# Performance work log

Measured on AMD Instinct MI355X. Metric: run time of the kernel, lower is better.

The kernel has to match this reference:

```python
import jax, jax.numpy as jnp
import numpy as np

N = 50000   # nodes
E = 400000  # directed edges (line-graph nodes)
LE = 1600000  # line-graph edges
B = 256     # graphs in batch
F = 64      # n_feats
ED = 16     # edge_dim
NIT = 3     # n_iter
SF = 6 * F  # LinearBlock hidden


def _seg_softmax(vals, seg, num):
    # numerically stable segment softmax (PyG softmax)
    m = jax.ops.segment_max(vals, seg, num_segments=num)
    e = jnp.exp(vals - m[seg])
    s = jax.ops.segment_sum(e, seg, num_segments=num)
    return e / (s[seg] + 1e-16)


def _gat_pool(out, lg_src, lg_dst, batch, gat_W, att_src, att_dst, gat_bias):
    # PyG GATConv(F, 1): heads=1, add_self_loops=True, negative_slope=0.2
    xw = out @ gat_W                       # [E, 1]
    sl = jnp.arange(E, dtype=lg_src.dtype)
    src = jnp.concatenate([lg_src, sl])
    dst = jnp.concatenate([lg_dst, sl])
    a_s = xw[:, 0] * att_src[0]
    a_d = xw[:, 0] * att_dst[0]
    alpha = jax.nn.leaky_relu(a_s[src] + a_d[dst], negative_slope=0.2)
    coef = _seg_softmax(alpha, dst, E)     # softmax over incoming line-edges
    xc = jax.ops.segment_sum(coef[:, None] * xw[src], dst, num_segments=E) + gat_bias  # [E,1]
    # GlobalAttentionPool: segment softmax over batch, then weighted sum pool
    sc = _seg_softmax(xc[:, 0], batch, B)[:, None]
    return jax.ops.segment_sum(out * sc, batch, num_segments=B)  # [B, F]


def _bn(x, g, b):
    # BatchNorm1d in training mode (batch stats, biased var, eps=1e-5)
    m = x.mean(0)
    v = ((x - m) ** 2).mean(0)
    return (x - m) * jax.lax.rsqrt(v + 1e-5) * g + b


def _prelu(x, w):
    return jnp.where(x >= 0, x, w * x)


def _lin_block(x, bn1_g, bn1_b, W1, b1, bn_g, bn_b, pr, W, b, bn5_g, bn5_b, pr5, W5, b5):
    x = _bn(x, bn1_g, bn1_b) @ W1 + b1                       # lin1: [N, 6F]
    h = _prelu(_bn(x, bn_g[0], bn_b[0]), pr[0]) @ W[0] + b[0]  # lin2
    h = _prelu(_bn(h, bn_g[1], bn_b[1]), pr[1]) @ W[1] + b[1]  # lin3
    x = (h + x) / 2
    x = (_prelu(_bn(x, bn_g[2], bn_b[2]), pr[2]) @ W[2] + b[2] + x) / 2  # lin4
    x = _prelu(_bn(x, bn5_g, bn5_b), pr5) @ W5 + b5          # lin5: [N, F]
    return x


def setup_inputs() -> dict:
    key = jax.random.key(0)
    ks = jax.random.split(key, 20)
    def nrm(k, shape, s=0.1):
        return jax.random.normal(k, shape, jnp.float32) * s
    inp = {}
    inp["x"] = jax.random.normal(ks[0], (N, F), jnp.float32)
    inp["edge_attr"] = jax.random.normal(ks[1], (E, ED), jnp.float32)
    inp["edge_index"] = jax.random.randint(ks[2], (2, E), 0, N, jnp.int32)
    inp["line_graph_edge_index"] = jax.random.randint(ks[3], (2, LE), 0, E, jnp.int32)
    inp["edge_index_batch"] = jnp.sort(jax.random.randint(ks[4], (E,), 0, B, jnp.int32))
    inp["W_u"] = nrm(ks[5], (F, F)); inp["W_v"] = nrm(ks[6], (F, F)); inp["W_e"] = nrm(ks[7], (ED, F))
    inp["gat_W"] = nrm(ks[8], (F, 1)); inp["gat_att_src"] = nrm(ks[9], (1,)); inp["gat_att_dst"] = nrm(ks[10], (1,))
    inp["gat_bias"] = jnp.zeros((1,), jnp.float32)
    inp["a"] = nrm(ks[11], (1, F, NIT)); inp["a_bias"] = jnp.zeros((1, 1, NIT), jnp.float32)
    inp["W_gout"] = nrm(ks[12], (F, F)); inp["b_gout"] = jnp.zeros((F,), jnp.float32)
    inp["lb_bn1_g"] = jnp.ones((F,), jnp.float32); inp["lb_bn1_b"] = jnp.zeros((F,), jnp.float32)
    inp["lb_W1"] = nrm(ks[13], (F, SF)); inp["lb_b1"] = jnp.zeros((SF,), jnp.float32)
    inp["lb_bn_g"] = jnp.ones((3, SF), jnp.float32); inp["lb_bn_b"] = jnp.zeros((3, SF), jnp.float32)
    inp["lb_pr"] = jnp.full((3,), 0.25, jnp.float32)
    inp["lb_W"] = nrm(ks[14], (3, SF, SF)); inp["lb_b"] = jnp.zeros((3, SF), jnp.float32)
    inp["lb_bn5_g"] = jnp.ones((SF,), jnp.float32); inp["lb_bn5_b"] = jnp.zeros((SF,), jnp.float32)
    inp["lb_pr5"] = jnp.array(0.25, jnp.float32)
    inp["lb_W5"] = nrm(ks[15], (SF, F)); inp["lb_b5"] = jnp.zeros((F,), jnp.float32)
    return inp


def reference(x, edge_attr, W_u, W_v, W_e, gat_W, gat_att_src, gat_att_dst, gat_bias,
              a, a_bias, W_gout, b_gout,
              lb_bn1_g, lb_bn1_b, lb_W1, lb_b1, lb_bn_g, lb_bn_b, lb_pr, lb_W, lb_b,
              lb_bn5_g, lb_bn5_b, lb_pr5, lb_W5, lb_b5,
              edge_index, line_graph_edge_index, edge_index_batch):
    ei0, ei1 = edge_index[0], edge_index[1]
    lg0, lg1 = line_graph_edge_index[0], line_graph_edge_index[1]
    # initial directed-edge features
    ea = ((x @ W_u)[ei0] + (x @ W_v)[ei1] + edge_attr @ W_e) / 3.0  # [E, F]
    out = ea
    outs, gouts = [], []
    for _ in range(NIT):
        out = ea + jax.ops.segment_sum(out[lg0], lg1, num_segments=E)  # line-graph message passing
        gout = _gat_pool(out, lg0, lg1, edge_index_batch, gat_W, gat_att_src, gat_att_dst, gat_bias)
        outs.append(out)
        gouts.append(jnp.tanh(gout @ W_gout + b_gout))
    out_all = jnp.stack(outs, -1)    # [E, F, NIT]
    gout_all = jnp.stack(gouts, -1)  # [B, F, NIT]
    sc = jax.nn.softmax((gout_all * a).sum(1, keepdims=True) + a_bias, axis=-1)  # [B,1,NIT]
    out = (out_all * sc[edge_index_batch]).sum(-1)  # per-edge gather == repeat_interleave(degree)
    xn = x + jax.ops.segment_sum(out, ei1, num_segments=N)
    return _lin_block(xn, lb_bn1_g, lb_bn1_b, lb_W1, lb_b1, lb_bn_g, lb_bn_b, lb_pr, lb_W, lb_b,
                      lb_bn5_g, lb_bn5_b, lb_pr5, lb_W5, lb_b5)
```

## Files before the change

kernel.cpp:

```cpp
#include <hip/hip_runtime.h>
#include <math.h>

#define NN 50000
#define EE 400000
#define LEE 1600000
#define BBATCH 256
#define FF 64
#define EDD 16
#define NITER 3
#define SFD 384

#define CDIV(a,b) (((a)+(b)-1)/(b))

typedef unsigned short ushort_t;
typedef __attribute__((ext_vector_type(8))) short bf16x8;
typedef __attribute__((ext_vector_type(4))) float f32x4;

__device__ inline float b2f(ushort_t u) { return __uint_as_float(((unsigned)u) << 16); }
__device__ inline ushort_t f2b(float f) {
    unsigned u = __float_as_uint(f);
    return (ushort_t)((u + 0x7fffu + ((u >> 16) & 1u)) >> 16);
}

__global__ void k_hist(const int* __restrict__ idx, int n, int* __restrict__ cnt) {
    int i = blockIdx.x * blockDim.x + threadIdx.x;
    if (i < n) atomicAdd(&cnt[idx[i]], 1);
}
__global__ void k_part(const int* __restrict__ in, int n, int* __restrict__ part) {
    __shared__ int s[256];
    int i = blockIdx.x * 256 + threadIdx.x;
    s[threadIdx.x] = (i < n) ? in[i] : 0;
    __syncthreads();
    for (int off = 128; off > 0; off >>= 1) {
        if (threadIdx.x < off) s[threadIdx.x] += s[threadIdx.x + off];
        __syncthreads();
    }
    if (threadIdx.x == 0) part[blockIdx.x] = s[0];
}
__global__ void k_scan_single(int* __restrict__ a, int n) {
    __shared__ int s[256];
    int v = (threadIdx.x < n) ? a[threadIdx.x] : 0;
    s[threadIdx.x] = v; __syncthreads();
    for (int off = 1; off < 256; off <<= 1) {
        int t = (threadIdx.x >= off) ? s[threadIdx.x - off] : 0;
        __syncthreads(); s[threadIdx.x] += t; __syncthreads();
    }
    if (threadIdx.x < n) a[threadIdx.x] = s[threadIdx.x] - v;
}
__global__ void k_scan_add(int* __restrict__ a, int n, const int* __restrict__ off) {
    __shared__ int s[256];
    int i = blockIdx.x * 256 + threadIdx.x;
    int v = (i < n) ? a[i] : 0;
    s[threadIdx.x] = v; __syncthreads();
    for (int o = 1; o < 256; o <<= 1) {
        int t = (threadIdx.x >= o) ? s[threadIdx.x - o] : 0;
        __syncthreads(); s[threadIdx.x] += t; __syncthreads();
    }
    if (i < n) a[i] = s[threadIdx.x] - v + off[blockIdx.x];
}
__global__ void k_scan_out(const int* __restrict__ in, int n, const int* __restrict__ boff,
                           int* __restrict__ out) {
    __shared__ int s[256];
    int i = blockIdx.x * 256 + threadIdx.x;
    int v = (i < n) ? in[i] : 0;
    s[threadIdx.x] = v; __syncthreads();
    for (int o = 1; o < 256; o <<= 1) {
        int t = (threadIdx.x >= o) ? s[threadIdx.x - o] : 0;
        __syncthreads(); s[threadIdx.x] += t; __syncthreads();
    }
    if (i < n) out[i] = s[threadIdx.x] - v + boff[blockIdx.x];
    if (i == n - 1) out[n] = s[threadIdx.x] + boff[blockIdx.x];
}
__global__ void k_fill_lg(const int* __restrict__ lg, const int* __restrict__ rowptr,
                          int* __restrict__ cnt, int* __restrict__ srcidx) {
    int i = blockIdx.x * blockDim.x + threadIdx.x;
    if (i >= LEE) return;
    int d = lg[LEE + i];
    int pos = rowptr[d] + atomicAdd(&cnt[d], 1);
    srcidx[pos] = lg[i];
}
__global__ void k_fill_n(const int* __restrict__ ei, const int* __restrict__ rowptr,
                         int* __restrict__ cnt, int* __restrict__ nidx) {
    int i = blockIdx.x * blockDim.x + threadIdx.x;
    if (i >= EE) return;
    int d = ei[EE + i];
    int pos = rowptr[d] + atomicAdd(&cnt[d], 1);
    nidx[pos] = i;
}


__global__ void k_node_mm(const float* __restrict__ x, const float* __restrict__ Wu,
                          const float* __restrict__ Wv, ushort_t* __restrict__ xu,
                          ushort_t* __restrict__ xv) {
    __shared__ float su[64 * 64];
    __shared__ float sv[64 * 64];
    int tid = threadIdx.x;
    for (int i = tid; i < 64 * 64; i += blockDim.x) { su[i] = Wu[i]; sv[i] = Wv[i]; }
    __syncthreads();
    int row = blockIdx.x * 4 + (tid >> 6);
    int f = tid & 63;
    if (row >= NN) return;
    const float* xr = x + (long long)row * 64;
    float au = 0.f, av = 0.f;
    #pragma unroll
    for (int k = 0; k < 64; ++k) {
        float xv_ = xr[k];
        au += xv_ * su[k * 64 + f];
        av += xv_ * sv[k * 64 + f];
    }
    xu[(long long)row * 64 + f] = f2b(au);
    xv[(long long)row * 64 + f] = f2b(av);
}

__global__ void k_ea_b16(const ushort_t* __restrict__ xu, const ushort_t* __restrict__ xv,
                         const float* __restrict__ eattr, const float* __restrict__ We,
                         const int* __restrict__ ei, ushort_t* __restrict__ eab) {
    __shared__ float swe[16 * 64];
    int tid = threadIdx.x;
    for (int i = tid; i < 1024; i += 256) swe[i] = We[i];
    __syncthreads();
    int e = blockIdx.x * 8 + (tid >> 5);
    int f2 = (tid & 31) * 2;
    if (e >= EE) return;
    int s = ei[e];
    int d = ei[EE + e];
    unsigned us = *(const unsigned*)&xu[(long long)s * 64 + f2];
    unsigned ud = *(const unsigned*)&xv[(long long)d * 64 + f2];
    const float* ar = eattr + (long long)e * 16;
    float a0 = 0.f, a1 = 0.f;
    #pragma unroll
    for (int k = 0; k < 16; ++k) {
        float w = ar[k];
        a0 += w * swe[k * 64 + f2];
        a1 += w * swe[k * 64 + f2 + 1];
    }
    float v0 = (b2f((ushort_t)us) + b2f((ushort_t)ud) + a0) * (1.0f / 3.0f);
    float v1 = (b2f((ushort_t)(us >> 16)) + b2f((ushort_t)(ud >> 16)) + a1) * (1.0f / 3.0f);
    *(unsigned*)&eab[(long long)e * 64 + f2] = (unsigned)f2b(v0) | ((unsigned)f2b(v1) << 16);
}

__global__ void k_mp_gather(const ushort_t* __restrict__ prev,
                            const ushort_t* __restrict__ eab,
                            const int* __restrict__ rowptr, const int* __restrict__ srcidx,
                            const float* __restrict__ gatW,
                            ushort_t* __restrict__ outb, float* __restrict__ xw) {
    int tid = threadIdx.x;
    int d = blockIdx.x * 8 + (tid >> 5);
    int f2 = (tid & 31) * 2;
    if (d >= EE) return;
    unsigned ue = *(const unsigned*)&eab[(long long)d * 64 + f2];
    float a0 = b2f((ushort_t)ue), a1 = b2f((ushort_t)(ue >> 16));
    int p0 = rowptr[d], p1 = rowptr[d + 1];
    int j = p0;
    for (; j + 4 <= p1; j += 4) {
        int s0 = srcidx[j], s1 = srcidx[j + 1], s2 = srcidx[j + 2], s3 = srcidx[j + 3];
        unsigned u0 = *(const unsigned*)&prev[(long long)s0 * 64 + f2];
        unsigned u1 = *(const unsigned*)&prev[(long long)s1 * 64 + f2];
        unsigned u2 = *(const unsigned*)&prev[(long long)s2 * 64 + f2];
        unsigned u3 = *(const unsigned*)&prev[(long long)s3 * 64 + f2];
        a0 += (b2f((ushort_t)u0) + b2f((ushort_t)u1)) + (b2f((ushort_t)u2) + b2f((ushort_t)u3));
        a1 += (b2f((ushort_t)(u0 >> 16)) + b2f((ushort_t)(u1 >> 16))) +
              (b2f((ushort_t)(u2 >> 16)) + b2f((ushort_t)(u3 >> 16)));
    }
    for (; j < p1; ++j) {
        unsigned u0 = *(const unsigned*)&prev[(long long)srcidx[j] * 64 + f2];
        a0 += b2f((ushort_t)u0);
        a1 += b2f((ushort_t)(u0 >> 16));
    }
    *(unsigned*)&outb[(long long)d * 64 + f2] = (unsigned)f2b(a0) | ((unsigned)f2b(a1) << 16);
    float w = a0 * gatW[f2] + a1 * gatW[f2 + 1];
    #pragma unroll
    for (int o = 16; o > 0; o >>= 1) w += __shfl_down(w, o, 32);
    if ((tid & 31) == 0) xw[d] = w;
}

__global__ void k_gat_fused(const float* __restrict__ xw,
                            const int* __restrict__ rowptr, const int* __restrict__ srcidx,
                            const float* __restrict__ att_s, const float* __restrict__ att_d,
                            const float* __restrict__ gbias, float* __restrict__ xc) {
    int e = blockIdx.x * blockDim.x + threadIdx.x;
    if (e >= EE) return;
    float as = att_s[0], ad = att_d[0];
    float xwd = xw[e];
    float adt = xwd * ad;
    float aself = xwd * as + adt;
    if (aself < 0.f) aself *= 0.2f;
    int p0 = rowptr[e], p1 = rowptr[e + 1];
    float m = aself;
    for (int j = p0; j < p1; ++j) {
        float a = xw[srcidx[j]] * as + adt;
        if (a < 0.f) a *= 0.2f;
        m = fmaxf(m, a);
    }
    float ssum = expf(aself - m);
    float wsum = ssum * xwd;
    for (int j = p0; j < p1; ++j) {
        float xs = xw[srcidx[j]];
        float a = xs * as + adt;
        if (a < 0.f) a *= 0.2f;
        float ev = expf(a - m);
        ssum += ev;
        wsum += ev * xs;
    }
    xc[e] = wsum / (ssum + 1e-16f) + gbias[0];
}

__global__ void k_batchptr(const int* __restrict__ batch, int* __restrict__ bptr) {
    int e = blockIdx.x * blockDim.x + threadIdx.x;
    if (e >= EE) return;
    int b = batch[e];
    int bp = (e == 0) ? -1 : batch[e - 1];
    for (int q = bp + 1; q <= b; ++q) bptr[q] = e;
    if (e == EE - 1)
        for (int q = b + 1; q <= BBATCH; ++q) bptr[q] = EE;
}

__global__ void k_pool(const float* __restrict__ xc, const ushort_t* __restrict__ out,
                       const int* __restrict__ bptr, float* __restrict__ gout) {
    int b = blockIdx.x;
    int p0 = bptr[b], p1 = bptr[b + 1];
    __shared__ float red[256];
    int tid = threadIdx.x;
    float mx = -INFINITY;
    for (int e = p0 + tid; e < p1; e += 256) mx = fmaxf(mx, xc[e]);
    red[tid] = mx; __syncthreads();
    for (int s = 128; s > 0; s >>= 1) { if (tid < s) red[tid] = fmaxf(red[tid], red[tid + s]); __syncthreads(); }
    float m = red[0]; __syncthreads();
    float sm = 0.f;
    for (int e = p0 + tid; e < p1; e += 256) sm += expf(xc[e] - m);
    red[tid] = sm; __syncthreads();
    for (int s = 128; s > 0; s >>= 1) { if (tid < s) red[tid] += red[tid + s]; __syncthreads(); }
    float ssum = red[0] + 1e-16f; __syncthreads();
    int f = tid & 63, chunk = tid >> 6;
    float acc = 0.f;
    for (int e = p0 + chunk; e < p1; e += 4) {
        float w = expf(xc[e] - m);
        acc += w * b2f(out[(long long)e * 64 + f]);
    }
    red[tid] = acc; __syncthreads();
    if (chunk == 0) {
        float tot = red[f] + red[64 + f] + red[128 + f] + red[192 + f];
        gout[b * 64 + f] = tot / ssum;
    }
}

__global__ void k_gout_mm(const float* __restrict__ gout, const float* __restrict__ Wg,
                          const float* __restrict__ bg, float* __restrict__ gt) {
    __shared__ float sw[64 * 64];
    int tid = threadIdx.x;
    for (int i = tid; i < 4096; i += blockDim.x) sw[i] = Wg[i];
    __syncthreads();
    int row = blockIdx.x * 4 + (tid >> 6);
    int f = tid & 63;
    if (row >= BBATCH) return;
    const float* gr = gout + row * 64;
    float acc = bg[f];
    #pragma unroll
    for (int k = 0; k < 64; ++k) acc += gr[k] * sw[k * 64 + f];
    gt[row * 64 + f] = tanhf(acc);
}

__global__ void k_att(const float* __restrict__ g0, const float* __restrict__ g1,
                      const float* __restrict__ g2, const float* __restrict__ a,
                      const float* __restrict__ abias, float* __restrict__ sc) {
    int b = blockIdx.x;
    int f = threadIdx.x;
    float v0 = g0[b * 64 + f] * a[f * 3 + 0];
    float v1 = g1[b * 64 + f] * a[f * 3 + 1];
    float v2 = g2[b * 64 + f] * a[f * 3 + 2];
    #pragma unroll
    for (int o = 32; o > 0; o >>= 1) {
        v0 += __shfl_down(v0, o, 64);
        v1 += __shfl_down(v1, o, 64);
        v2 += __shfl_down(v2, o, 64);
    }
    if (f == 0) {
        float s0 = v0 + abias[0], s1 = v1 + abias[1], s2 = v2 + abias[2];
        float m = fmaxf(s0, fmaxf(s1, s2));
        float e0 = expf(s0 - m), e1 = expf(s1 - m), e2 = expf(s2 - m);
        float inv = 1.0f / (e0 + e1 + e2);
        sc[b * 3 + 0] = e0 * inv; sc[b * 3 + 1] = e1 * inv; sc[b * 3 + 2] = e2 * inv;
    }
}

__global__ void k_comb(ushort_t* __restrict__ o1, const ushort_t* __restrict__ o2,
                       const ushort_t* __restrict__ o3, const float* __restrict__ sc,
                       const int* __restrict__ batch) {
    long long idx = (long long)blockIdx.x * blockDim.x + threadIdx.x;
    if (idx >= (long long)EE * 64) return;
    int e = (int)(idx >> 6);
    int b = batch[e];
    float v = b2f(o1[idx]) * sc[b * 3] + b2f(o2[idx]) * sc[b * 3 + 1] + b2f(o3[idx]) * sc[b * 3 + 2];
    o1[idx] = f2b(v);
}

__global__ void k_node_gather(const ushort_t* __restrict__ comb, const int* __restrict__ nrow,
                              const int* __restrict__ nidx, const float* __restrict__ x,
                              ushort_t* __restrict__ xnb) {
    int tid = threadIdx.x;
    int n = blockIdx.x * 4 + (tid >> 6);
    int f = tid & 63;
    if (n >= NN) return;
    float acc = x[(long long)n * 64 + f];
    int p0 = nrow[n], p1 = nrow[n + 1];
    int j = p0;
    for (; j + 4 <= p1; j += 4) {
        int e0 = nidx[j], e1 = nidx[j + 1], e2 = nidx[j + 2], e3 = nidx[j + 3];
        float v0 = b2f(comb[(long long)e0 * 64 + f]);
        float v1 = b2f(comb[(long long)e1 * 64 + f]);
        float v2 = b2f(comb[(long long)e2 * 64 + f]);
        float v3 = b2f(comb[(long long)e3 * 64 + f]);
        acc += (v0 + v1) + (v2 + v3);
    }
    for (; j < p1; ++j) acc += b2f(comb[(long long)nidx[j] * 64 + f]);
    xnb[(long long)n * 64 + f] = f2b(acc);
}

__global__ void k_colstats_b16(const ushort_t* __restrict__ X, int ncols, int nrows,
                               float* __restrict__ csum, float* __restrict__ csumsq) {
    int c = threadIdx.x;
    int rpb = CDIV(nrows, (int)gridDim.x);
    int r0 = blockIdx.x * rpb;
    int r1 = min(r0 + rpb, nrows);
    float s = 0.f, s2 = 0.f;
    for (int r = r0; r < r1; ++r) {
        float v = b2f(X[(long long)r * ncols + c]);
        s += v; s2 += v * v;
    }
    atomicAdd(&csum[c], s);
    atomicAdd(&csumsq[c], s2);
}

__global__ void k_wtrans(const float* __restrict__ W, int K, int M, ushort_t* __restrict__ Wt) {
    __shared__ ushort_t tile[32][33];
    int kb = blockIdx.y * 32, mb = blockIdx.x * 32;
    int tx = threadIdx.x & 31, ty = threadIdx.x >> 5;
    for (int dy = ty; dy < 32; dy += 8) {
        int k = kb + dy, m = mb + tx;
        tile[dy][tx] = (k < K && m < M) ? f2b(W[(long long)k * M + m]) : (ushort_t)0;
    }
    __syncthreads();
    for (int dy = ty; dy < 32; dy += 8) {
        int m = mb + dy, k = kb + tx;
        if (m < M && k < K) Wt[(long long)m * K + k] = tile[tx][dy];
    }
}

template<int KK, int WR, int WC>
__global__ __launch_bounds__(256) void k_gemm_fused(
    const ushort_t* __restrict__ A, const ushort_t* __restrict__ Wt,
    const float* __restrict__ bias, const ushort_t* __restrict__ resb,
    const float* __restrict__ csum, const float* __restrict__ csumsq,
    const float* __restrict__ g, const float* __restrict__ bb,
    const float* __restrict__ pr, float scale, int nrows, int M,
    ushort_t* __restrict__ Cb, float* __restrict__ Cf,
    float* __restrict__ osum, float* __restrict__ osumsq) {
    constexpr int RT = WR * 64;
    __shared__ ushort_t sA[RT][36];
    __shared__ float sScl[KK], sOff[KK];
    int tid = threadIdx.x;
    int wave = tid >> 6, lane = tid & 63;
    int l16 = lane & 15, klo = lane >> 4;
    int wrow = wave / WC, wcol = wave % WC;
    long long rowBase = (long long)blockIdx.x * RT;
    int colBase = blockIdx.y * (WC * 64);
    float prs = pr ? pr[0] : 1.0f;
    const float invn = 1.0f / (float)NN;
    for (int c = tid; c < KK; c += 256) {
        float mean = csum[c] * invn;
        float var = csumsq[c] * invn - mean * mean;
        float scl = rsqrtf(var + 1e-5f) * g[c];
        sScl[c] = scl;
        sOff[c] = bb[c] - mean * scl;
    }
    __syncthreads();
    f32x4 acc[4][4] = {};
    for (int k0 = 0; k0 < KK; k0 += 32) {
        #pragma unroll
        for (int it = 0; it < RT * 32 / (256 * 8); ++it) {
            int idx = (it * 256 + tid) * 8;
            int r = idx >> 5, kk = idx & 31;
            long long gr = rowBase + r;
            uint4 raw = {0u, 0u, 0u, 0u};
            if (gr < nrows) raw = *(const uint4*)&A[gr * KK + k0 + kk];
            unsigned outw[4];
            #pragma unroll
            for (int q = 0; q < 4; ++q) {
                unsigned rw = ((const unsigned*)&raw)[q];
                int c = k0 + kk + q * 2;
                float t0 = b2f((ushort_t)rw) * sScl[c] + sOff[c];
                float t1 = b2f((ushort_t)(rw >> 16)) * sScl[c + 1] + sOff[c + 1];
                if (t0 < 0.f) t0 *= prs;
                if (t1 < 0.f) t1 *= prs;
                outw[q] = (unsigned)f2b(t0) | ((unsigned)f2b(t1) << 16);
            }
            uint2 w0; w0.x = outw[0]; w0.y = outw[1];
            uint2 w1; w1.x = outw[2]; w1.y = outw[3];
            *(uint2*)&sA[r][kk] = w0;
            *(uint2*)&sA[r][kk + 4] = w1;
        }
        __syncthreads();
        bf16x8 bfr[4];
        #pragma unroll
        for (int n = 0; n < 4; ++n) {
            int col = colBase + wcol * 64 + n * 16 + l16;
            bfr[n] = *(const bf16x8*)&Wt[(long long)col * KK + k0 + klo * 8];
        }
        bf16x8 afr[4];
        #pragma unroll
        for (int m = 0; m < 4; ++m) {
            union { uint2 p[2]; bf16x8 v; } u;
            int row = wrow * 64 + m * 16 + l16;
            u.p[0] = *(const uint2*)&sA[row][klo * 8];
            u.p[1] = *(const uint2*)&sA[row][klo * 8 + 4];
            afr[m] = u.v;
        }
        #pragma unroll
        for (int m = 0; m < 4; ++m)
            #pragma unroll
            for (int n = 0; n < 4; ++n)
                acc[m][n] = __builtin_amdgcn_mfma_f32_16x16x32_bf16(afr[m], bfr[n], acc[m][n], 0, 0, 0);
        __syncthreads();
    }
    #pragma unroll
    for (int m = 0; m < 4; ++m) {
        #pragma unroll
        for (int n = 0; n < 4; ++n) {
            int col = colBase + wcol * 64 + n * 16 + l16;
            long long row0 = rowBase + wrow * 64 + m * 16 + klo * 4;
            float bcol = bias[col];
            float s = 0.f, s2 = 0.f;
            #pragma unroll
            for (int r = 0; r < 4; ++r) {
                long long row = row0 + r;
                if (row < nrows) {
                    float v = acc[m][n][r] + bcol;
                    if (resb) v += b2f(resb[row * M + col]);
                    v *= scale;
                    if (Cf) Cf[row * M + col] = v;
                    if (Cb) Cb[row * M + col] = f2b(v);
                    s += v; s2 += v * v;
                }
            }
            if (osum) {
                s += __shfl_down(s, 32, 64);
                s2 += __shfl_down(s2, 32, 64);
                s += __shfl_down(s, 16, 64);
                s2 += __shfl_down(s2, 16, 64);
                if (lane < 16) {
                    atomicAdd(&osum[col], s);
                    atomicAdd(&osumsq[col], s2);
                }
            }
        }
    }
}

extern "C" void kernel_launch(void* const* d_in, const int* in_sizes, int n_in,
                              void* d_out, int out_size, void* d_ws, size_t ws_size,
                              hipStream_t stream) {
    const float* x       = (const float*)d_in[0];
    const float* eattr   = (const float*)d_in[1];
    const int*   ei      = (const int*)d_in[2];
    const int*   lg      = (const int*)d_in[3];
    const int*   batch   = (const int*)d_in[4];
    const float* W_u     = (const float*)d_in[5];
    const float* W_v     = (const float*)d_in[6];
    const float* W_e     = (const float*)d_in[7];
    const float* gat_W   = (const float*)d_in[8];
    const float* att_s   = (const float*)d_in[9];
    const float* att_d   = (const float*)d_in[10];
    const float* gat_b   = (const float*)d_in[11];
    const float* a_att   = (const float*)d_in[12];
    const float* a_bias  = (const float*)d_in[13];
    const float* W_gout  = (const float*)d_in[14];
    const float* b_gout  = (const float*)d_in[15];
    const float* bn1_g   = (const float*)d_in[16];
    const float* bn1_b   = (const float*)d_in[17];
    const float* lb_W1   = (const float*)d_in[18];
    const float* lb_b1   = (const float*)d_in[19];
    const float* lb_bn_g = (const float*)d_in[20];
    const float* lb_bn_b = (const float*)d_in[21];
    const float* lb_pr   = (const float*)d_in[22];
    const float* lb_W    = (const float*)d_in[23];
    const float* lb_b    = (const float*)d_in[24];
    const float* bn5_g   = (const float*)d_in[25];
    const float* bn5_b   = (const float*)d_in[26];
    const float* pr5     = (const float*)d_in[27];
    const float* lb_W5   = (const float*)d_in[28];
    const float* lb_b5   = (const float*)d_in[29];
    float* out_final = (float*)d_out;

    const long long ESZ = (long long)EE * FF;
    const long long NSZ = (long long)NN * FF;
    char* cur = (char*)d_ws;
    auto alloc = [&](size_t bytes) -> void* {
        void* p = (void*)cur;
        cur += (bytes + 255) & ~(size_t)255;
        return p;
    };
    ushort_t* XU = (ushort_t*)alloc(NSZ * 2);
    ushort_t* XV = (ushort_t*)alloc(NSZ * 2);
    ushort_t* O1 = (ushort_t*)alloc(ESZ * 2);
    ushort_t* O2 = (ushort_t*)alloc(ESZ * 2);
    ushort_t* O3 = (ushort_t*)alloc(ESZ * 2);
    float* XW = (float*)alloc((size_t)EE * 4);
    float* XC = (float*)alloc((size_t)EE * 4);
    ushort_t* XNB = (ushort_t*)alloc(NSZ * 2);
    float* GRAW = (float*)alloc(BBATCH * FF * 4);
    float* G0 = (float*)alloc(BBATCH * FF * 4);
    float* G1 = (float*)alloc(BBATCH * FF * 4);
    float* G2 = (float*)alloc(BBATCH * FF * 4);
    float* SCATT = (float*)alloc(BBATCH * 3 * 4);
    int* BPTR = (int*)alloc((BBATCH + 1) * 4);
    int* LROW = (int*)alloc((size_t)(EE + 1) * 4);
    int* LSRC = (int*)alloc((size_t)LEE * 4);
    int* LCNT = (int*)alloc((size_t)EE * 4);
    int* NROW = (int*)alloc((size_t)(NN + 1) * 4);
    int* NIDX = (int*)alloc((size_t)EE * 4);
    int* NCNT = (int*)alloc((size_t)NN * 4);
    int* SP0 = (int*)alloc(2048 * 4);
    int* SP1 = (int*)alloc(256 * 4);
    float* STATS = (float*)alloc(5 * 2 * SFD * 4);
    ushort_t* WT1 = (ushort_t*)alloc((size_t)SFD * FF * 2);
    ushort_t* WT2 = (ushort_t*)alloc((size_t)SFD * SFD * 2);
    ushort_t* WT3 = (ushort_t*)alloc((size_t)SFD * SFD * 2);
    ushort_t* WT4 = (ushort_t*)alloc((size_t)SFD * SFD * 2);
    ushort_t* WT5 = (ushort_t*)alloc((size_t)FF * SFD * 2);
    if ((size_t)(cur - (char*)d_ws) > ws_size) return;

    ushort_t* T1B = O1;
    ushort_t* T2B = T1B + (long long)NN * SFD;
    ushort_t* T3B = T2B + (long long)NN * SFD;
    ushort_t* T4B = T3B + (long long)NN * SFD;
    float* CS[5][2];
    for (int i = 0; i < 5; ++i) { CS[i][0] = STATS + i * 2 * SFD; CS[i][1] = CS[i][0] + SFD; }
    float* GTS[3] = {G0, G1, G2};

    hipMemsetAsync(STATS, 0, 5 * 2 * SFD * 4, stream);

    {
        dim3 gt(SFD / 32, FF / 32);
        k_wtrans<<<gt, 256, 0, stream>>>(lb_W1, FF, SFD, WT1);
        dim3 gs(SFD / 32, SFD / 32);
        k_wtrans<<<gs, 256, 0, stream>>>(lb_W, SFD, SFD, WT2);
        k_wtrans<<<gs, 256, 0, stream>>>(lb_W + (long long)SFD * SFD, SFD, SFD, WT3);
        k_wtrans<<<gs, 256, 0, stream>>>(lb_W + 2LL * SFD * SFD, SFD, SFD, WT4);
        dim3 g5(FF / 32, SFD / 32);
        k_wtrans<<<g5, 256, 0, stream>>>(lb_W5, SFD, FF, WT5);
    }

    k_node_mm<<<CDIV(NN, 4), 256, 0, stream>>>(x, W_u, W_v, XU, XV);
    k_batchptr<<<CDIV(EE, 256), 256, 0, stream>>>(batch, BPTR);

    {
        hipMemsetAsync(LCNT, 0, (size_t)EE * 4, stream);
        k_hist<<<CDIV(LEE, 256), 256, 0, stream>>>(lg + LEE, LEE, LCNT);
        int nb0 = CDIV(EE, 256), nb1 = CDIV(nb0, 256);
        k_part<<<nb0, 256, 0, stream>>>(LCNT, EE, SP0);
        k_part<<<nb1, 256, 0, stream>>>(SP0, nb0, SP1);
        k_scan_single<<<1, 256, 0, stream>>>(SP1, nb1);
        k_scan_add<<<nb1, 256, 0, stream>>>(SP0, nb0, SP1);
        k_scan_out<<<nb0, 256, 0, stream>>>(LCNT, EE, SP0, LROW);
        hipMemsetAsync(LCNT, 0, (size_t)EE * 4, stream);
        k_fill_lg<<<CDIV(LEE, 256), 256, 0, stream>>>(lg, LROW, LCNT, LSRC);
    }
    {
        hipMemsetAsync(NCNT, 0, (size_t)NN * 4, stream);
        k_hist<<<CDIV(EE, 256), 256, 0, stream>>>(ei + EE, EE, NCNT);
        int nb0 = CDIV(NN, 256), nb1 = CDIV(nb0, 256);
        k_part<<<nb0, 256, 0, stream>>>(NCNT, NN, SP0);
        k_part<<<nb1, 256, 0, stream>>>(SP0, nb0, SP1);
        k_scan_single<<<1, 256, 0, stream>>>(SP1, nb1);
        k_scan_add<<<nb1, 256, 0, stream>>>(SP0, nb0, SP1);
        k_scan_out<<<nb0, 256, 0, stream>>>(NCNT, NN, SP0, NROW);
        hipMemsetAsync(NCNT, 0, (size_t)NN * 4, stream);
        k_fill_n<<<CDIV(EE, 256), 256, 0, stream>>>(ei, NROW, NCNT, NIDX);
    }

    const int EB8 = CDIV(EE, 8);

    auto gat_pool = [&](ushort_t* buf, int t) {
        k_gat_fused<<<CDIV(EE, 256), 256, 0, stream>>>(XW, LROW, LSRC, att_s, att_d, gat_b, XC);
        k_pool<<<BBATCH, 256, 0, stream>>>(XC, buf, BPTR, GRAW);
        k_gout_mm<<<CDIV(BBATCH, 4), 256, 0, stream>>>(GRAW, W_gout, b_gout, GTS[t]);
    };

    k_ea_b16<<<EB8, 256, 0, stream>>>(XU, XV, eattr, W_e, ei, O3);
    k_mp_gather<<<EB8, 256, 0, stream>>>(O3, O3, LROW, LSRC, gat_W, O1, XW);
    gat_pool(O1, 0);
    k_mp_gather<<<EB8, 256, 0, stream>>>(O1, O3, LROW, LSRC, gat_W, O2, XW);
    gat_pool(O2, 1);
    k_mp_gather<<<EB8, 256, 0, stream>>>(O2, O3, LROW, LSRC, gat_W, O3, XW);
    gat_pool(O3, 2);

    k_att<<<BBATCH, 64, 0, stream>>>(G0, G1, G2, a_att, a_bias, SCATT);
    k_comb<<<(int)CDIV(ESZ, 256), 256, 0, stream>>>(O1, O2, O3, SCATT, batch);
    k_node_gather<<<CDIV(NN, 4), 256, 0, stream>>>(O1, NROW, NIDX, x, XNB);
    k_colstats_b16<<<256, FF, 0, stream>>>(XNB, FF, NN, CS[0][0], CS[0][1]);

    {
        dim3 g(CDIV(NN, 128), SFD / 128);
        k_gemm_fused<64, 2, 2><<<g, 256, 0, stream>>>(XNB, WT1, lb_b1, nullptr,
            CS[0][0], CS[0][1], bn1_g, bn1_b, nullptr, 1.0f, NN, SFD,
            T1B, nullptr, CS[1][0], CS[1][1]);
        k_gemm_fused<384, 2, 2><<<g, 256, 0, stream>>>(T1B, WT2, lb_b, nullptr,
            CS[1][0], CS[1][1], lb_bn_g, lb_bn_b, lb_pr, 1.0f, NN, SFD,
            T2B, nullptr, CS[2][0], CS[2][1]);
        k_gemm_fused<384, 2, 2><<<g, 256, 0, stream>>>(T2B, WT3, lb_b + SFD, T1B,
            CS[2][0], CS[2][1], lb_bn_g + SFD, lb_bn_b + SFD, lb_pr + 1, 0.5f, NN, SFD,
            T3B, nullptr, CS[3][0], CS[3][1]);
        k_gemm_fused<384, 2, 2><<<g, 256, 0, stream>>>(T3B, WT4, lb_b + 2 * SFD, T3B,
            CS[3][0], CS[3][1], lb_bn_g + 2 * SFD, lb_bn_b + 2 * SFD, lb_pr + 2, 0.5f, NN, SFD,
            T4B, nullptr, CS[4][0], CS[4][1]);
        dim3 g5(CDIV(NN, 256), 1);
        k_gemm_fused<384, 4, 1><<<g5, 256, 0, stream>>>(T4B, WT5, lb_b5, nullptr,
            CS[4][0], CS[4][1], bn5_g, bn5_b, pr5, 1.0f, NN, FF,
            nullptr, out_final, nullptr, nullptr);
    }
}
```

Before: 2.082 ms.

## Cover full output width per block in fused MLP GEMMs to avoid redundant A prep

Reworks the fused BN+PReLU GEMM so that each 512-thread block computes all output columns (384) for a 128-row tile, instead of splitting columns across three blocks. Each A tile is then loaded from global memory and normalized/activated once rather than three times. The tile shape is templated, and the final 64-column GEMM uses 8 waves over 256 rows. The cost is fewer blocks (about 391), larger per-wave accumulators (4x6 fragments) and 512-thread blocks, which may lower occupancy and raise register pressure.

```diff
diff --git a/kernel.cpp b/kernel.cpp
--- a/kernel.cpp
+++ b/kernel.cpp
@@ -346,16 +346,19 @@
     }
 }
 
-template<int KK, int WR, int WC>
-__global__ __launch_bounds__(256) void k_gemm_fused(
+template<int KK, int MT, int WR, int WC, int RT>
+__global__ __launch_bounds__(512) void k_gemm_fused(
     const ushort_t* __restrict__ A, const ushort_t* __restrict__ Wt,
     const float* __restrict__ bias, const ushort_t* __restrict__ resb,
     const float* __restrict__ csum, const float* __restrict__ csumsq,
     const float* __restrict__ g, const float* __restrict__ bb,
-    const float* __restrict__ pr, float scale, int nrows, int M,
+    const float* __restrict__ pr, float scale, int nrows,
     ushort_t* __restrict__ Cb, float* __restrict__ Cf,
     float* __restrict__ osum, float* __restrict__ osumsq) {
-    constexpr int RT = WR * 64;
+    constexpr int RTW = RT / WR;
+    constexpr int MTW = MT / WC;
+    constexpr int FM = RTW / 16;
+    constexpr int FN = MTW / 16;
     __shared__ ushort_t sA[RT][36];
     __shared__ float sScl[KK], sOff[KK];
     int tid = threadIdx.x;
@@ -363,10 +366,9 @@
     int l16 = lane & 15, klo = lane >> 4;
     int wrow = wave / WC, wcol = wave % WC;
     long long rowBase = (long long)blockIdx.x * RT;
-    int colBase = blockIdx.y * (WC * 64);
     float prs = pr ? pr[0] : 1.0f;
     const float invn = 1.0f / (float)NN;
-    for (int c = tid; c < KK; c += 256) {
+    for (int c = tid; c < KK; c += 512) {
         float mean = csum[c] * invn;
         float var = csumsq[c] * invn - mean * mean;
         float scl = rsqrtf(var + 1e-5f) * g[c];
@@ -374,11 +376,11 @@
         sOff[c] = bb[c] - mean * scl;
     }
     __syncthreads();
-    f32x4 acc[4][4] = {};
+    f32x4 acc[FM][FN] = {};
     for (int k0 = 0; k0 < KK; k0 += 32) {
         #pragma unroll
-        for (int it = 0; it < RT * 32 / (256 * 8); ++it) {
-            int idx = (it * 256 + tid) * 8;
+        for (int it = 0; it < RT * 32 / (512 * 8); ++it) {
+            int idx = (it * 512 + tid) * 8;
             int r = idx >> 5, kk = idx & 31;
             long long gr = rowBase + r;
             uint4 raw = {0u, 0u, 0u, 0u};
@@ -400,34 +402,34 @@
             *(uint2*)&sA[r][kk + 4] = w1;
         }
         __syncthreads();
-        bf16x8 bfr[4];
+        bf16x8 bfr[FN];
         #pragma unroll
-        for (int n = 0; n < 4; ++n) {
-            int col = colBase + wcol * 64 + n * 16 + l16;
+        for (int n = 0; n < FN; ++n) {
+            int col = wcol * MTW + n * 16 + l16;
             bfr[n] = *(const bf16x8*)&Wt[(long long)col * KK + k0 + klo * 8];
         }
-        bf16x8 afr[4];
+        bf16x8 afr[FM];
         #pragma unroll
-        for (int m = 0; m < 4; ++m) {
+        for (int m = 0; m < FM; ++m) {
             union { uint2 p[2]; bf16x8 v; } u;
-            int row = wrow * 64 + m * 16 + l16;
+            int row = wrow * RTW + m * 16 + l16;
             u.p[0] = *(const uint2*)&sA[row][klo * 8];
             u.p[1] = *(const uint2*)&sA[row][klo * 8 + 4];
             afr[m] = u.v;
         }
         #pragma unroll
-        for (int m = 0; m < 4; ++m)
+        for (int m = 0; m < FM; ++m)
             #pragma unroll
-            for (int n = 0; n < 4; ++n)
+            for (int n = 0; n < FN; ++n)
                 acc[m][n] = __builtin_amdgcn_mfma_f32_16x16x32_bf16(afr[m], bfr[n], acc[m][n], 0, 0, 0);
         __syncthreads();
     }
     #pragma unroll
-    for (int m = 0; m < 4; ++m) {
+    for (int m = 0; m < FM; ++m) {
         #pragma unroll
-        for (int n = 0; n < 4; ++n) {
-            int col = colBase + wcol * 64 + n * 16 + l16;
-            long long row0 = rowBase + wrow * 64 + m * 16 + klo * 4;
+        for (int n = 0; n < FN; ++n) {
+            int col = wcol * MTW + n * 16 + l16;
+            long long row0 = rowBase + wrow * RTW + m * 16 + klo * 4;
             float bcol = bias[col];
             float s = 0.f, s2 = 0.f;
             #pragma unroll
@@ -435,10 +437,10 @@
                 long long row = row0 + r;
                 if (row < nrows) {
                     float v = acc[m][n][r] + bcol;
-                    if (resb) v += b2f(resb[row * M + col]);
+                    if (resb) v += b2f(resb[row * MT + col]);
                     v *= scale;
-                    if (Cf) Cf[row * M + col] = v;
-                    if (Cb) Cb[row * M + col] = f2b(v);
+                    if (Cf) Cf[row * MT + col] = v;
+                    if (Cb) Cb[row * MT + col] = f2b(v);
                     s += v; s2 += v * v;
                 }
             }
@@ -600,22 +602,21 @@
     k_colstats_b16<<<256, FF, 0, stream>>>(XNB, FF, NN, CS[0][0], CS[0][1]);
 
     {
-        dim3 g(CDIV(NN, 128), SFD / 128);
-        k_gemm_fused<64, 2, 2><<<g, 256, 0, stream>>>(XNB, WT1, lb_b1, nullptr,
-            CS[0][0], CS[0][1], bn1_g, bn1_b, nullptr, 1.0f, NN, SFD,
+        const int GB128 = CDIV(NN, 128);
+        k_gemm_fused<64, 384, 2, 4, 128><<<GB128, 512, 0, stream>>>(XNB, WT1, lb_b1, nullptr,
+            CS[0][0], CS[0][1], bn1_g, bn1_b, nullptr, 1.0f, NN,
             T1B, nullptr, CS[1][0], CS[1][1]);
-        k_gemm_fused<384, 2, 2><<<g, 256, 0, stream>>>(T1B, WT2, lb_b, nullptr,
-            CS[1][0], CS[1][1], lb_bn_g, lb_bn_b, lb_pr, 1.0f, NN, SFD,
+        k_gemm_fused<384, 384, 2, 4, 128><<<GB128, 512, 0, stream>>>(T1B, WT2, lb_b, nullptr,
+            CS[1][0], CS[1][1], lb_bn_g, lb_bn_b, lb_pr, 1.0f, NN,
             T2B, nullptr, CS[2][0], CS[2][1]);
-        k_gemm_fused<384, 2, 2><<<g, 256, 0, stream>>>(T2B, WT3, lb_b + SFD, T1B,
-            CS[2][0], CS[2][1], lb_bn_g + SFD, lb_bn_b + SFD, lb_pr + 1, 0.5f, NN, SFD,
+        k_gemm_fused<384, 384, 2, 4, 128><<<GB128, 512, 0, stream>>>(T2B, WT3, lb_b + SFD, T1B,
+            CS[2][0], CS[2][1], lb_bn_g + SFD, lb_bn_b + SFD, lb_pr + 1, 0.5f, NN,
             T3B, nullptr, CS[3][0], CS[3][1]);
-        k_gemm_fused<384, 2, 2><<<g, 256, 0, stream>>>(T3B, WT4, lb_b + 2 * SFD, T3B,
-            CS[3][0], CS[3][1], lb_bn_g + 2 * SFD, lb_bn_b + 2 * SFD, lb_pr + 2, 0.5f, NN, SFD,
+        k_gemm_fused<384, 384, 2, 4, 128><<<GB128, 512, 0, stream>>>(T3B, WT4, lb_b + 2 * SFD, T3B,
+            CS[3][0], CS[3][1], lb_bn_g + 2 * SFD, lb_bn_b + 2 * SFD, lb_pr + 2, 0.5f, NN,
             T4B, nullptr, CS[4][0], CS[4][1]);
-        dim3 g5(CDIV(NN, 256), 1);
-        k_gemm_fused<384, 4, 1><<<g5, 256, 0, stream>>>(T4B, WT5, lb_b5, nullptr,
-            CS[4][0], CS[4][1], bn5_g, bn5_b, pr5, 1.0f, NN, FF,
+        k_gemm_fused<384, 64, 8, 1, 256><<<CDIV(NN, 256), 512, 0, stream>>>(T4B, WT5, lb_b5, nullptr,
+            CS[4][0], CS[4][1], bn5_g, bn5_b, pr5, 1.0f, NN,
             nullptr, out_final, nullptr, nullptr);
     }
 }
```

Result: faster. 1.998 ms (-4.0%).
